# Kernel tuning notes

Hardware: AMD Instinct MI355X
Metric: run time of the kernel (lower is better)

## Reference

```python
import jax, jax.numpy as jnp
import numpy as np

B, N, D = 4, 2048, 512
H, DH = 8, 64
MLP = 2048
EPS = 1e-5


def setup_inputs() -> dict:
    key = jax.random.key(0)
    ks = jax.random.split(key, 8)
    s = lambda fan_in: 1.0 / np.sqrt(fan_in)
    return {
        "x": jax.random.normal(ks[0], (B, N, D), jnp.float32),
        "ln1_g": jnp.ones((D,), jnp.float32),
        "ln1_b": jnp.zeros((D,), jnp.float32),
        "Wqkv": jax.random.normal(ks[1], (D, 3 * H * DH), jnp.float32) * s(D),
        "temperature": jnp.asarray(np.log(DH ** -0.5), jnp.float32),
        "Wo": jax.random.normal(ks[2], (H * DH, D), jnp.float32) * s(H * DH),
        "bo": jnp.zeros((D,), jnp.float32),
        "ln2_g": jnp.ones((D,), jnp.float32),
        "ln2_b": jnp.zeros((D,), jnp.float32),
        "W1": jax.random.normal(ks[3], (D, MLP), jnp.float32) * s(D),
        "b1": jnp.zeros((MLP,), jnp.float32),
        "W2": jax.random.normal(ks[4], (MLP, D), jnp.float32) * s(MLP),
        "b2": jnp.zeros((D,), jnp.float32),
    }


def _layernorm(x, g, b):
    mu = jnp.mean(x, axis=-1, keepdims=True)
    var = jnp.var(x, axis=-1, keepdims=True)
    return (x - mu) * jax.lax.rsqrt(var + EPS) * g + b


def _lsa(x, Wqkv, temperature, Wo, bo):
    b, n, _ = x.shape
    qkv = x @ Wqkv  # [b, n, 3*H*DH]
    q, k, v = jnp.split(qkv, 3, axis=-1)
    rs = lambda t: t.reshape(b, n, H, DH).transpose(0, 2, 1, 3)  # b h n d
    q, k, v = rs(q), rs(k), rs(v)
    dots = jnp.einsum("bhnd,bhmd->bhnm", q, k) * jnp.exp(temperature)
    mask_value = -jnp.finfo(dots.dtype).max
    eye = jnp.eye(n, dtype=bool)
    dots = jnp.where(eye, mask_value, dots)  # mask diagonal (LSA)
    attn = jax.nn.softmax(dots, axis=-1)
    out = jnp.einsum("bhnm,bhmd->bhnd", attn, v)
    out = out.transpose(0, 2, 1, 3).reshape(b, n, H * DH)
    return out @ Wo + bo


def _ffn(x, W1, b1, W2, b2):
    h = jax.nn.gelu(x @ W1 + b1, approximate=False)
    return h @ W2 + b2


def reference(x, ln1_g, ln1_b, Wqkv, temperature, Wo, bo,
              ln2_g, ln2_b, W1, b1, W2, b2):
    y = _lsa(_layernorm(x, ln1_g, ln1_b), Wqkv, temperature, Wo, bo) + x
    z = _ffn(_layernorm(y, ln2_g, ln2_b), W1, b1, W2, b2) + y
    return (z, x)
```

## Files before the change

### kernel.cpp

```cpp
#include <hip/hip_runtime.h>
#include <math.h>

typedef __attribute__((ext_vector_type(4))) float f32x4;
typedef __attribute__((ext_vector_type(8))) short short8;

#define DEV __device__ __forceinline__

DEV short f2bf(float f){
  union { float f; unsigned u; } v; v.f = f;
  unsigned r = v.u + 0x7fffu + ((v.u >> 16) & 1u);
  return (short)(r >> 16);
}
DEV float bf2f(short s){
  union { unsigned u; float f; } v; v.u = ((unsigned)(unsigned short)s) << 16; return v.f;
}
DEV float exp2_hw(float x){ float r; asm("v_exp_f32 %0, %1" : "=v"(r) : "v"(x)); return r; }
DEV float rcp_hw(float x){ float r; asm("v_rcp_f32 %0, %1" : "=v"(r) : "v"(x)); return r; }
DEV unsigned cvtpk(float a, float b){
  unsigned r; asm("v_cvt_pk_bf16_f32 %0, %1, %2" : "=v"(r) : "v"(a), "v"(b)); return r;
}
DEV void gload_lds16(const short* src, short* lds){
  __builtin_amdgcn_global_load_lds(
      (const __attribute__((address_space(1))) void*)src,
      (__attribute__((address_space(3))) void*)lds, 16, 0, 0);
}

__global__ __launch_bounds__(256) void transpose_bf16_kernel(
    const float* __restrict__ W, short* __restrict__ Wt, int K, int N)
{
  __shared__ float tile[32][33];
  int nb = blockIdx.x * 32, kb = blockIdx.y * 32;
  int tx = threadIdx.x & 31, ty = threadIdx.x >> 5;
  #pragma unroll
  for (int i = ty; i < 32; i += 8)
    tile[i][tx] = W[(size_t)(kb + i) * N + nb + tx];
  __syncthreads();
  #pragma unroll
  for (int i = ty; i < 32; i += 8)
    Wt[(size_t)(nb + i) * K + kb + tx] = f2bf(tile[tx][i]);
}

template<int COPYX>
__global__ __launch_bounds__(256) void ln_kernel(
    const float* __restrict__ x, const float* __restrict__ g,
    const float* __restrict__ b, short* __restrict__ out,
    float* __restrict__ xcopy)
{
  int row  = blockIdx.x * 4 + (threadIdx.x >> 6);
  int lane = threadIdx.x & 63;
  const float* xr = x + (size_t)row * 512 + lane * 8;
  f32x4 v0 = *(const f32x4*)(xr);
  f32x4 v1 = *(const f32x4*)(xr + 4);
  float s  = (v0[0]+v0[1]+v0[2]+v0[3]) + (v1[0]+v1[1]+v1[2]+v1[3]);
  float sq = (v0[0]*v0[0]+v0[1]*v0[1]+v0[2]*v0[2]+v0[3]*v0[3])
           + (v1[0]*v1[0]+v1[1]*v1[1]+v1[2]*v1[2]+v1[3]*v1[3]);
  #pragma unroll
  for (int off = 1; off < 64; off <<= 1) {
    s  += __shfl_xor(s, off);
    sq += __shfl_xor(sq, off);
  }
  float mu  = s * (1.0f / 512.0f);
  float var = sq * (1.0f / 512.0f) - mu * mu;
  float rstd = rsqrtf(var + 1e-5f);
  f32x4 g0 = *(const f32x4*)(g + lane * 8);
  f32x4 g1 = *(const f32x4*)(g + lane * 8 + 4);
  f32x4 b0 = *(const f32x4*)(b + lane * 8);
  f32x4 b1 = *(const f32x4*)(b + lane * 8 + 4);
  float o[8];
  #pragma unroll
  for (int j = 0; j < 4; ++j) o[j]     = (v0[j] - mu) * rstd * g0[j] + b0[j];
  #pragma unroll
  for (int j = 0; j < 4; ++j) o[4 + j] = (v1[j] - mu) * rstd * g1[j] + b1[j];
  uint4 pk;
  pk.x = cvtpk(o[0], o[1]); pk.y = cvtpk(o[2], o[3]);
  pk.z = cvtpk(o[4], o[5]); pk.w = cvtpk(o[6], o[7]);
  *(uint4*)(out + (size_t)row * 512 + lane * 8) = pk;
  if (COPYX) {
    float* xc = xcopy + (size_t)row * 512 + lane * 8;
    *(f32x4*)(xc)     = v0;
    *(f32x4*)(xc + 4) = v1;
  }
}

template<int EPI, int BM, typename OutT>
__global__ __launch_bounds__(256) void gemm_bt_kernel(
    const short* __restrict__ A, const short* __restrict__ Bt,
    OutT* __restrict__ C, const float* __restrict__ bias,
    const float* __restrict__ resid, short* __restrict__ vt,
    int M, int N, int K)
{
  constexpr int MFR = BM / 32;
  constexpr int NFR = 4;
  constexpr int AI  = BM / 64;
  constexpr int BUF = BM * 32 + 128 * 32;
  __shared__ __align__(16) short smem[3 * BUF];

  int tid = threadIdx.x;
  int lane = tid & 63, wid = tid >> 6;
  int l16 = lane & 15, lq = lane >> 4;

  int gx = gridDim.x;
  int nwg = gx * gridDim.y;
  int orig = blockIdx.y * gx + blockIdx.x;
  int swz = (orig & 7) * (nwg >> 3) + (orig >> 3);
  int bn = swz % gx, bm = swz / gx;

  int wm = wid >> 1, wn = wid & 1;

  const short* gaP[AI];
  const short* gbP[2];
  #pragma unroll
  for (int i = 0; i < AI; ++i) {
    int gg = i * 4 + wid;
    gaP[i] = A + (size_t)(bm * BM + gg * 16 + l16) * K + lq * 8;
  }
  #pragma unroll
  for (int i = 0; i < 2; ++i) {
    int gg = i * 4 + wid;
    gbP[i] = Bt + (size_t)(bn * 128 + gg * 16 + l16) * K + lq * 8;
  }

  auto STAGE = [&](int bufi, int k0) {
    short* base = smem + bufi * BUF;
    #pragma unroll
    for (int i = 0; i < AI; ++i)
      gload_lds16(gaP[i] + k0, base + (i * 4 + wid) * 512);
    #pragma unroll
    for (int i = 0; i < 2; ++i)
      gload_lds16(gbP[i] + k0, base + BM * 32 + (i * 4 + wid) * 512);
  };

  f32x4 acc[MFR][NFR] = {};

  STAGE(0, 0);
  STAGE(1, 32);

  int nt = K >> 5;
  for (int t = 0; t < nt; ++t) {
    if (t + 1 < nt) {
      if constexpr (AI == 2) asm volatile("s_waitcnt vmcnt(4)" ::: "memory");
      else                   asm volatile("s_waitcnt vmcnt(3)" ::: "memory");
    } else {
      asm volatile("s_waitcnt vmcnt(0)" ::: "memory");
    }
    __builtin_amdgcn_s_barrier();
    __builtin_amdgcn_sched_barrier(0);
    if (t + 2 < nt) STAGE((t + 2) % 3, (t + 2) << 5);

    const short* base = smem + (t % 3) * BUF;
    short8 af[MFR], bfr[NFR];
    #pragma unroll
    for (int m = 0; m < MFR; ++m)
      af[m] = *(const short8*)(base + (wm * MFR + m) * 512 + lane * 8);
    #pragma unroll
    for (int n = 0; n < NFR; ++n)
      bfr[n] = *(const short8*)(base + BM * 32 + (wn * NFR + n) * 512 + lane * 8);
    __builtin_amdgcn_s_setprio(1);
    #pragma unroll
    for (int m = 0; m < MFR; ++m)
      #pragma unroll
      for (int n = 0; n < NFR; ++n)
        acc[m][n] = __builtin_amdgcn_mfma_f32_16x16x32_bf16(af[m], bfr[n], acc[m][n], 0, 0, 0);
    __builtin_amdgcn_s_setprio(0);
  }

  if (EPI == 3 && bn >= 8) {
    __syncthreads();
    short* T = smem;
    #pragma unroll
    for (int m = 0; m < MFR; ++m)
      #pragma unroll
      for (int n = 0; n < NFR; ++n) {
        int c = wn * 64 + n * 16 + l16;
        #pragma unroll
        for (int r = 0; r < 4; ++r) {
          int rowl = wm * 64 + m * 16 + lq * 4 + r;
          T[c * 128 + (rowl ^ ((c & 7) << 4))] = f2bf(acc[m][n][r]);
        }
      }
    __syncthreads();
    int b2 = bm >> 4;
    int nnb = (bm & 15) * 128;
    int tn = tid & 15;
    #pragma unroll
    for (int c8 = 0; c8 < 8; ++c8) {
      int c = c8 * 16 + (tid >> 4);
      short8 v = *(const short8*)(T + c * 128 + ((tn * 8) ^ ((c & 7) << 4)));
      if (tn & 1) {
        short8 w;
        #pragma unroll
        for (int j = 0; j < 8; ++j) w[j] = v[j ^ 4];
        v = w;
      }
      int c2 = bn * 128 + c - 1024;
      int bh = b2 * 8 + (c2 >> 6);
      int d  = c2 & 63;
      *(short8*)(vt + ((size_t)(bh * 64 + d)) * 2048 + nnb + tn * 8) = v;
    }
    return;
  }

  float bv[NFR];
  #pragma unroll
  for (int n = 0; n < NFR; ++n)
    bv[n] = (EPI == 0 || EPI == 3) ? 0.0f : bias[bn * 128 + (wn * NFR + n) * 16 + l16];

  #pragma unroll
  for (int m = 0; m < MFR; ++m) {
    #pragma unroll
    for (int r = 0; r < 4; ++r) {
      int row = bm * BM + (wm * MFR + m) * 16 + lq * 4 + r;
      #pragma unroll
      for (int n = 0; n < NFR; ++n) {
        int col = bn * 128 + (wn * NFR + n) * 16 + l16;
        float v = acc[m][n][r];
        if (EPI == 1 || EPI == 2) v += bv[n];
        if (EPI == 2) v = 0.5f * v * (1.0f + erff(v * 0.70710678f));
        if (EPI == 1) v += resid[(size_t)row * N + col];
        if constexpr (sizeof(OutT) == 2)
          ((short*)C)[(size_t)row * N + col] = f2bf(v);
        else
          ((float*)C)[(size_t)row * N + col] = v;
      }
    }
  }
}

__global__ __launch_bounds__(256, 2) void attn_kernel(
    const short* __restrict__ qkv, const short* __restrict__ vt,
    const float* __restrict__ temp_ptr, short* __restrict__ out)
{
  __shared__ __align__(16) short smem[24576];

  int tid = threadIdx.x;
  int lane = tid & 63, wid = tid >> 6;
  int l16 = lane & 15, lq = lane >> 4;
  int hi = lq >> 1, lq0 = lq & 1;

  int orig = blockIdx.y * 16 + blockIdx.x;
  int swz = (orig & 7) * 64 + (orig >> 3);
  int qb = swz & 15, bh = swz >> 4;
  int b = bh >> 3, h = bh & 7;

  const short* qbase = qkv + (size_t)b * 2048 * 1536 + h * 64;
  const short* kbase = qbase + 512;
  const short* vbase = vt + (size_t)bh * 64 * 2048;

  float scale = __expf(temp_ptr[0]) * 1.44269504f;
  int q0 = qb * 128 + wid * 32;

  short8 qfrag[2][2];
  #pragma unroll
  for (int qf = 0; qf < 2; ++qf) {
    int qrow = q0 + qf * 16 + l16;
    #pragma unroll
    for (int c = 0; c < 2; ++c) {
      short8 raw = *(const short8*)(qbase + (size_t)qrow * 1536 + c * 32 + lq * 8);
      short8 sc;
      #pragma unroll
      for (int j = 0; j < 8; ++j) sc[j] = f2bf(bf2f(raw[j]) * scale);
      qfrag[qf][c] = sc;
    }
  }

  f32x4 accO[2][4] = {};
  float l[2] = {0.f, 0.f};

  auto STAGE = [&](int bufi, int k0) {
    #pragma unroll
    for (int i = 0; i < 2; ++i) {
      int w16 = i * 256 + tid;
      int sub = w16 >> 7;
      int cc  = (w16 >> 6) & 1;
      int lq2 = (w16 >> 4) & 3;
      int l2  = w16 & 15;
      const short* srcK = kbase + (size_t)(k0 + sub * 16 + l2) * 1536 + cc * 32 + lq2 * 8;
      gload_lds16(srcK, smem + bufi * 4096 + (i * 4 + wid) * 512);
      const short* srcV = vbase + (size_t)(sub * 16 + l2) * 2048 + k0 + cc * 32 + lq2 * 8;
      gload_lds16(srcV, smem + 12288 + bufi * 4096 + (i * 4 + wid) * 512);
    }
  };

  STAGE(0, 0);
  STAGE(1, 64);

  for (int t = 0; t < 32; ++t) {
    if (t + 1 < 32) asm volatile("s_waitcnt vmcnt(4)" ::: "memory");
    else            asm volatile("s_waitcnt vmcnt(0)" ::: "memory");
    __builtin_amdgcn_s_barrier();
    __builtin_amdgcn_sched_barrier(0);
    if (t + 2 < 32) STAGE((t + 2) % 3, (t + 2) * 64);

    int k0 = t * 64;
    const short* kls = smem + (t % 3) * 4096;
    const short* vls = smem + 12288 + (t % 3) * 4096;

    f32x4 accS[2][4] = {};
    __builtin_amdgcn_s_setprio(1);
    #pragma unroll
    for (int s = 0; s < 4; ++s) {
      short8 kf0 = *(const short8*)(kls + (s * 2 + 0) * 512 + lane * 8);
      short8 kf1 = *(const short8*)(kls + (s * 2 + 1) * 512 + lane * 8);
      #pragma unroll
      for (int qf = 0; qf < 2; ++qf) {
        accS[qf][s] = __builtin_amdgcn_mfma_f32_16x16x32_bf16(kf0, qfrag[qf][0], accS[qf][s], 0, 0, 0);
        accS[qf][s] = __builtin_amdgcn_mfma_f32_16x16x32_bf16(kf1, qfrag[qf][1], accS[qf][s], 0, 0, 0);
      }
    }
    __builtin_amdgcn_s_setprio(0);

    if ((q0 & ~63) == k0) {
      #pragma unroll
      for (int qf = 0; qf < 2; ++qf) {
        int qg = q0 + qf * 16 + l16;
        #pragma unroll
        for (int s = 0; s < 4; ++s)
          #pragma unroll
          for (int r = 0; r < 4; ++r)
            if (k0 + s * 16 + lq * 4 + r == qg) accS[qf][s][r] = -30000.f;
      }
    }

    short8 pa[2][2];
    #pragma unroll
    for (int qf = 0; qf < 2; ++qf) {
      float sum = 0.f;
      unsigned W[4][2];
      #pragma unroll
      for (int s = 0; s < 4; ++s) {
        float p0 = exp2_hw(accS[qf][s][0]);
        float p1 = exp2_hw(accS[qf][s][1]);
        float p2 = exp2_hw(accS[qf][s][2]);
        float p3 = exp2_hw(accS[qf][s][3]);
        sum += (p0 + p1) + (p2 + p3);
        W[s][0] = cvtpk(p0, p1);
        W[s][1] = cvtpk(p2, p3);
      }
      sum += __shfl_xor(sum, 16);
      sum += __shfl_xor(sum, 32);
      l[qf] += sum;

      unsigned K0[2], S0[2], K2[2], S2[2], R0[2], R2[2];
      #pragma unroll
      for (int w = 0; w < 2; ++w) {
        K0[w] = hi ? W[1][w] : W[0][w];
        S0[w] = hi ? W[0][w] : W[1][w];
        K2[w] = hi ? W[3][w] : W[2][w];
        S2[w] = hi ? W[2][w] : W[3][w];
      }
      #pragma unroll
      for (int w = 0; w < 2; ++w) {
        R0[w] = (unsigned)__shfl_xor((int)S0[w], 32);
        R2[w] = (unsigned)__shfl_xor((int)S2[w], 32);
      }
      bool sw = (hi != lq0);
      unsigned FA[2], FB[2], sA[2], sB[2], GA[2], GB[2];
      #pragma unroll
      for (int w = 0; w < 2; ++w) {
        sA[w] = sw ? K0[w] : R0[w];  FA[w] = sw ? R0[w] : K0[w];
        sB[w] = sw ? K2[w] : R2[w];  FB[w] = sw ? R2[w] : K2[w];
      }
      #pragma unroll
      for (int w = 0; w < 2; ++w) {
        GA[w] = (unsigned)__shfl_xor((int)sA[w], 16);
        GB[w] = (unsigned)__shfl_xor((int)sB[w], 16);
      }
      union { unsigned u[4]; short8 s8; } p0u, p1u;
      p0u.u[0] = FA[0]; p0u.u[1] = FA[1]; p0u.u[2] = GA[0]; p0u.u[3] = GA[1];
      p1u.u[0] = FB[0]; p1u.u[1] = FB[1]; p1u.u[2] = GB[0]; p1u.u[3] = GB[1];
      pa[qf][0] = p0u.s8;
      pa[qf][1] = p1u.s8;
    }

    short8 vfr[4][2];
    #pragma unroll
    for (int d = 0; d < 4; ++d) {
      vfr[d][0] = *(const short8*)(vls + (d * 2 + 0) * 512 + lane * 8);
      vfr[d][1] = *(const short8*)(vls + (d * 2 + 1) * 512 + lane * 8);
    }
    __builtin_amdgcn_s_setprio(1);
    #pragma unroll
    for (int qf = 0; qf < 2; ++qf)
      #pragma unroll
      for (int d = 0; d < 4; ++d) {
        accO[qf][d] = __builtin_amdgcn_mfma_f32_16x16x32_bf16(vfr[d][0], pa[qf][0], accO[qf][d], 0, 0, 0);
        accO[qf][d] = __builtin_amdgcn_mfma_f32_16x16x32_bf16(vfr[d][1], pa[qf][1], accO[qf][d], 0, 0, 0);
      }
    __builtin_amdgcn_s_setprio(0);
  }

  #pragma unroll
  for (int qf = 0; qf < 2; ++qf) {
    float inv = rcp_hw(l[qf]);
    int qg = q0 + qf * 16 + l16;
    size_t rowoff = (size_t)(b * 2048 + qg) * 512 + h * 64;
    #pragma unroll
    for (int d = 0; d < 4; ++d) {
      unsigned w0 = cvtpk(accO[qf][d][0] * inv, accO[qf][d][1] * inv);
      unsigned w1 = cvtpk(accO[qf][d][2] * inv, accO[qf][d][3] * inv);
      uint2 pk; pk.x = w0; pk.y = w1;
      *(uint2*)(out + rowoff + d * 16 + lq * 4) = pk;
    }
  }
}

extern "C" void kernel_launch(void* const* d_in, const int* in_sizes, int n_in,
                              void* d_out, int out_size, void* d_ws, size_t ws_size,
                              hipStream_t stream)
{
  const float* x    = (const float*)d_in[0];
  const float* ln1g = (const float*)d_in[1];
  const float* ln1b = (const float*)d_in[2];
  const float* Wqkv = (const float*)d_in[3];
  const float* temp = (const float*)d_in[4];
  const float* Wo   = (const float*)d_in[5];
  const float* bo   = (const float*)d_in[6];
  const float* ln2g = (const float*)d_in[7];
  const float* ln2b = (const float*)d_in[8];
  const float* W1   = (const float*)d_in[9];
  const float* b1   = (const float*)d_in[10];
  const float* W2   = (const float*)d_in[11];
  const float* b2   = (const float*)d_in[12];
  float* out = (float*)d_out;

  char* ws = (char*)d_ws;
  short* wqkv_t = (short*)(ws);
  short* wo_t   = (short*)(ws + 1572864);
  short* w1_t   = (short*)(ws + 2097152);
  short* w2_t   = (short*)(ws + 4194304);
  short* h      = (short*)(ws + 6291456);
  short* qkv    = (short*)(ws + 14680064);
  short* attn   = (short*)(ws + 39845888);
  float* y      = (float*)(ws + 48234496);
  short* vt     = (short*)(ws + 48234496);
  short* t      = (short*)(ws + 14680064);

  const int M = 8192;

  transpose_bf16_kernel<<<dim3(1536 / 32, 512 / 32),  256, 0, stream>>>(Wqkv, wqkv_t, 512, 1536);
  transpose_bf16_kernel<<<dim3(512 / 32, 512 / 32),   256, 0, stream>>>(Wo,   wo_t,   512, 512);
  transpose_bf16_kernel<<<dim3(2048 / 32, 512 / 32),  256, 0, stream>>>(W1,   w1_t,   512, 2048);
  transpose_bf16_kernel<<<dim3(512 / 32, 2048 / 32),  256, 0, stream>>>(W2,   w2_t,   2048, 512);

  ln_kernel<1><<<M / 4, 256, 0, stream>>>(x, ln1g, ln1b, h, out + (size_t)M * 512);

  gemm_bt_kernel<3, 128, short><<<dim3(1536 / 128, M / 128), 256, 0, stream>>>(
      h, wqkv_t, qkv, nullptr, nullptr, vt, M, 1536, 512);

  attn_kernel<<<dim3(16, 32), 256, 0, stream>>>(qkv, vt, temp, attn);

  gemm_bt_kernel<1, 64, float><<<dim3(512 / 128, M / 64), 256, 0, stream>>>(
      attn, wo_t, y, bo, x, nullptr, M, 512, 512);

  ln_kernel<0><<<M / 4, 256, 0, stream>>>(y, ln2g, ln2b, h, nullptr);

  gemm_bt_kernel<2, 128, short><<<dim3(2048 / 128, M / 128), 256, 0, stream>>>(
      h, w1_t, t, b1, nullptr, nullptr, M, 2048, 512);

  gemm_bt_kernel<1, 64, float><<<dim3(512 / 128, M / 64), 256, 0, stream>>>(
      t, w2_t, out, b2, y, nullptr, M, 512, 2048);
}
```

Before: 223.9 us.

## Split attention keys across two slices, use bf16 residual stream and tanh GELU

The attention kernel now splits the 2048 keys into two halves, doubling the grid. Each half writes unnormalized partial outputs and row sums, and a new combine kernel merges them. The intent is better CU occupancy, at the cost of an extra pass over the partial outputs and lower precision from rounding the partials to bf16. The post-attention residual y is also stored in bf16 instead of fp32, and LN2 reads the bf16 copy; this cuts memory traffic but loses precision. The exact erf GELU is replaced by a tanh approximation built on hardware exp and reciprocal, and the attention loop drops from triple to double buffering and no longer sets wave priority.

```diff
diff --git a/kernel.cpp b/kernel.cpp
--- a/kernel.cpp
+++ b/kernel.cpp
@@ -23,6 +23,12 @@
   __builtin_amdgcn_global_load_lds(
       (const __attribute__((address_space(1))) void*)src,
       (__attribute__((address_space(3))) void*)lds, 16, 0, 0);
+}
+DEV float gelu_fast(float v){
+  float u = v * (0.79788456f + 0.03567741f * v * v);
+  float e = exp2_hw(u * 2.88539008f);
+  float th = 1.0f - 2.0f * rcp_hw(e + 1.0f);
+  return 0.5f * v * (1.0f + th);
 }
 
 __global__ __launch_bounds__(256) void transpose_bf16_kernel(
@@ -82,12 +88,48 @@
   }
 }
 
+__global__ __launch_bounds__(256) void ln_bf_kernel(
+    const short* __restrict__ x, const float* __restrict__ g,
+    const float* __restrict__ b, short* __restrict__ out)
+{
+  int row  = blockIdx.x * 4 + (threadIdx.x >> 6);
+  int lane = threadIdx.x & 63;
+  short8 raw = *(const short8*)(x + (size_t)row * 512 + lane * 8);
+  float v[8];
+  #pragma unroll
+  for (int j = 0; j < 8; ++j) v[j] = bf2f(raw[j]);
+  float s = 0.f, sq = 0.f;
+  #pragma unroll
+  for (int j = 0; j < 8; ++j) { s += v[j]; sq += v[j] * v[j]; }
+  #pragma unroll
+  for (int off = 1; off < 64; off <<= 1) {
+    s  += __shfl_xor(s, off);
+    sq += __shfl_xor(sq, off);
+  }
+  float mu  = s * (1.0f / 512.0f);
+  float var = sq * (1.0f / 512.0f) - mu * mu;
+  float rstd = rsqrtf(var + 1e-5f);
+  f32x4 g0 = *(const f32x4*)(g + lane * 8);
+  f32x4 g1 = *(const f32x4*)(g + lane * 8 + 4);
+  f32x4 b0 = *(const f32x4*)(b + lane * 8);
+  f32x4 b1 = *(const f32x4*)(b + lane * 8 + 4);
+  float o[8];
+  #pragma unroll
+  for (int j = 0; j < 4; ++j) o[j]     = (v[j] - mu) * rstd * g0[j] + b0[j];
+  #pragma unroll
+  for (int j = 0; j < 4; ++j) o[4 + j] = (v[4+j] - mu) * rstd * g1[j] + b1[j];
+  uint4 pk;
+  pk.x = cvtpk(o[0], o[1]); pk.y = cvtpk(o[2], o[3]);
+  pk.z = cvtpk(o[4], o[5]); pk.w = cvtpk(o[6], o[7]);
+  *(uint4*)(out + (size_t)row * 512 + lane * 8) = pk;
+}
+
 template<int EPI, int BM, typename OutT>
 __global__ __launch_bounds__(256) void gemm_bt_kernel(
     const short* __restrict__ A, const short* __restrict__ Bt,
     OutT* __restrict__ C, const float* __restrict__ bias,
-    const float* __restrict__ resid, short* __restrict__ vt,
-    int M, int N, int K)
+    const float* __restrict__ resid, const short* __restrict__ residb,
+    short* __restrict__ vt, int M, int N, int K)
 {
   constexpr int MFR = BM / 32;
   constexpr int NFR = 4;
@@ -214,9 +256,10 @@
       for (int n = 0; n < NFR; ++n) {
         int col = bn * 128 + (wn * NFR + n) * 16 + l16;
         float v = acc[m][n][r];
-        if (EPI == 1 || EPI == 2) v += bv[n];
-        if (EPI == 2) v = 0.5f * v * (1.0f + erff(v * 0.70710678f));
-        if (EPI == 1) v += resid[(size_t)row * N + col];
+        if (EPI == 2 || EPI == 4 || EPI == 5) v += bv[n];
+        if (EPI == 2) v = gelu_fast(v);
+        if (EPI == 4) v += resid[(size_t)row * N + col];
+        if (EPI == 5) v += bf2f(residb[(size_t)row * N + col]);
         if constexpr (sizeof(OutT) == 2)
           ((short*)C)[(size_t)row * N + col] = f2bf(v);
         else
@@ -228,9 +271,10 @@
 
 __global__ __launch_bounds__(256, 2) void attn_kernel(
     const short* __restrict__ qkv, const short* __restrict__ vt,
-    const float* __restrict__ temp_ptr, short* __restrict__ out)
-{
-  __shared__ __align__(16) short smem[24576];
+    const float* __restrict__ temp_ptr,
+    short* __restrict__ Op0, short* __restrict__ Op1, float* __restrict__ Lbuf)
+{
+  __shared__ __align__(16) short smem[16384];
 
   int tid = threadIdx.x;
   int lane = tid & 63, wid = tid >> 6;
@@ -238,13 +282,16 @@
   int hi = lq >> 1, lq0 = lq & 1;
 
   int orig = blockIdx.y * 16 + blockIdx.x;
-  int swz = (orig & 7) * 64 + (orig >> 3);
-  int qb = swz & 15, bh = swz >> 4;
+  int swz = (orig & 7) * 128 + (orig >> 3);
+  int qb = swz & 15;
+  int rr = swz >> 4;
+  int bh = rr & 31, slice = rr >> 5;
   int b = bh >> 3, h = bh & 7;
 
   const short* qbase = qkv + (size_t)b * 2048 * 1536 + h * 64;
   const short* kbase = qbase + 512;
   const short* vbase = vt + (size_t)bh * 64 * 2048;
+  int kslice = slice * 1024;
 
   float scale = __expf(temp_ptr[0]) * 1.44269504f;
   int q0 = qb * 128 + wid * 32;
@@ -277,26 +324,23 @@
       const short* srcK = kbase + (size_t)(k0 + sub * 16 + l2) * 1536 + cc * 32 + lq2 * 8;
       gload_lds16(srcK, smem + bufi * 4096 + (i * 4 + wid) * 512);
       const short* srcV = vbase + (size_t)(sub * 16 + l2) * 2048 + k0 + cc * 32 + lq2 * 8;
-      gload_lds16(srcV, smem + 12288 + bufi * 4096 + (i * 4 + wid) * 512);
+      gload_lds16(srcV, smem + 8192 + bufi * 4096 + (i * 4 + wid) * 512);
     }
   };
 
-  STAGE(0, 0);
-  STAGE(1, 64);
-
-  for (int t = 0; t < 32; ++t) {
-    if (t + 1 < 32) asm volatile("s_waitcnt vmcnt(4)" ::: "memory");
-    else            asm volatile("s_waitcnt vmcnt(0)" ::: "memory");
-    __builtin_amdgcn_s_barrier();
-    __builtin_amdgcn_sched_barrier(0);
-    if (t + 2 < 32) STAGE((t + 2) % 3, (t + 2) * 64);
-
-    int k0 = t * 64;
-    const short* kls = smem + (t % 3) * 4096;
-    const short* vls = smem + 12288 + (t % 3) * 4096;
+  STAGE(0, kslice);
+  asm volatile("s_waitcnt vmcnt(0)");
+  __syncthreads();
+
+  for (int t = 0; t < 16; ++t) {
+    int cur = t & 1;
+    int k0 = kslice + t * 64;
+    if (t + 1 < 16) STAGE(cur ^ 1, k0 + 64);
+
+    const short* kls = smem + cur * 4096;
+    const short* vls = smem + 8192 + cur * 4096;
 
     f32x4 accS[2][4] = {};
-    __builtin_amdgcn_s_setprio(1);
     #pragma unroll
     for (int s = 0; s < 4; ++s) {
       short8 kf0 = *(const short8*)(kls + (s * 2 + 0) * 512 + lane * 8);
@@ -307,7 +351,6 @@
         accS[qf][s] = __builtin_amdgcn_mfma_f32_16x16x32_bf16(kf1, qfrag[qf][1], accS[qf][s], 0, 0, 0);
       }
     }
-    __builtin_amdgcn_s_setprio(0);
 
     if ((q0 & ~63) == k0) {
       #pragma unroll
@@ -378,7 +421,6 @@
       vfr[d][0] = *(const short8*)(vls + (d * 2 + 0) * 512 + lane * 8);
       vfr[d][1] = *(const short8*)(vls + (d * 2 + 1) * 512 + lane * 8);
     }
-    __builtin_amdgcn_s_setprio(1);
     #pragma unroll
     for (int qf = 0; qf < 2; ++qf)
       #pragma unroll
@@ -386,22 +428,48 @@
         accO[qf][d] = __builtin_amdgcn_mfma_f32_16x16x32_bf16(vfr[d][0], pa[qf][0], accO[qf][d], 0, 0, 0);
         accO[qf][d] = __builtin_amdgcn_mfma_f32_16x16x32_bf16(vfr[d][1], pa[qf][1], accO[qf][d], 0, 0, 0);
       }
-    __builtin_amdgcn_s_setprio(0);
-  }
-
+
+    __syncthreads();
+  }
+
+  short* op = slice ? Op1 : Op0;
   #pragma unroll
   for (int qf = 0; qf < 2; ++qf) {
-    float inv = rcp_hw(l[qf]);
     int qg = q0 + qf * 16 + l16;
+    if (lq == 0) Lbuf[(size_t)(slice * 32 + bh) * 2048 + qg] = l[qf];
     size_t rowoff = (size_t)(b * 2048 + qg) * 512 + h * 64;
     #pragma unroll
     for (int d = 0; d < 4; ++d) {
-      unsigned w0 = cvtpk(accO[qf][d][0] * inv, accO[qf][d][1] * inv);
-      unsigned w1 = cvtpk(accO[qf][d][2] * inv, accO[qf][d][3] * inv);
+      unsigned w0 = cvtpk(accO[qf][d][0], accO[qf][d][1]);
+      unsigned w1 = cvtpk(accO[qf][d][2], accO[qf][d][3]);
       uint2 pk; pk.x = w0; pk.y = w1;
-      *(uint2*)(out + rowoff + d * 16 + lq * 4) = pk;
-    }
-  }
+      *(uint2*)(op + rowoff + d * 16 + lq * 4) = pk;
+    }
+  }
+}
+
+__global__ __launch_bounds__(256) void attn_combine_kernel(
+    const short* __restrict__ Op0, const short* __restrict__ Op1,
+    const float* __restrict__ Lbuf, short* __restrict__ out)
+{
+  int idx = blockIdx.x * 256 + threadIdx.x;
+  size_t e = (size_t)idx * 8;
+  int row = (int)(e >> 9);
+  int col = (int)(e & 511);
+  int b = row >> 11, q = row & 2047;
+  int bh = b * 8 + (col >> 6);
+  float l0 = Lbuf[(size_t)bh * 2048 + q];
+  float l1 = Lbuf[(size_t)(32 + bh) * 2048 + q];
+  float inv = rcp_hw(l0 + l1);
+  short8 a = *(const short8*)(Op0 + e);
+  short8 c = *(const short8*)(Op1 + e);
+  float o[8];
+  #pragma unroll
+  for (int j = 0; j < 8; ++j) o[j] = (bf2f(a[j]) + bf2f(c[j])) * inv;
+  uint4 pk;
+  pk.x = cvtpk(o[0], o[1]); pk.y = cvtpk(o[2], o[3]);
+  pk.z = cvtpk(o[4], o[5]); pk.w = cvtpk(o[6], o[7]);
+  *(uint4*)(out + e) = pk;
 }
 
 extern "C" void kernel_launch(void* const* d_in, const int* in_sizes, int n_in,
@@ -425,13 +493,14 @@
 
   char* ws = (char*)d_ws;
   short* wqkv_t = (short*)(ws);
+  float* lpart  = (float*)(ws);
   short* wo_t   = (short*)(ws + 1572864);
   short* w1_t   = (short*)(ws + 2097152);
   short* w2_t   = (short*)(ws + 4194304);
   short* h      = (short*)(ws + 6291456);
   short* qkv    = (short*)(ws + 14680064);
   short* attn   = (short*)(ws + 39845888);
-  float* y      = (float*)(ws + 48234496);
+  short* ybf    = (short*)(ws + 48234496);
   short* vt     = (short*)(ws + 48234496);
   short* t      = (short*)(ws + 14680064);
 
@@ -445,18 +514,19 @@
   ln_kernel<1><<<M / 4, 256, 0, stream>>>(x, ln1g, ln1b, h, out + (size_t)M * 512);
 
   gemm_bt_kernel<3, 128, short><<<dim3(1536 / 128, M / 128), 256, 0, stream>>>(
-      h, wqkv_t, qkv, nullptr, nullptr, vt, M, 1536, 512);
-
-  attn_kernel<<<dim3(16, 32), 256, 0, stream>>>(qkv, vt, temp, attn);
-
-  gemm_bt_kernel<1, 64, float><<<dim3(512 / 128, M / 64), 256, 0, stream>>>(
-      attn, wo_t, y, bo, x, nullptr, M, 512, 512);
-
-  ln_kernel<0><<<M / 4, 256, 0, stream>>>(y, ln2g, ln2b, h, nullptr);
+      h, wqkv_t, qkv, nullptr, nullptr, nullptr, vt, M, 1536, 512);
+
+  attn_kernel<<<dim3(16, 64), 256, 0, stream>>>(qkv, vt, temp, attn, h, lpart);
+  attn_combine_kernel<<<M * 512 / 8 / 256, 256, 0, stream>>>(attn, h, lpart, attn);
+
+  gemm_bt_kernel<4, 64, short><<<dim3(512 / 128, M / 64), 256, 0, stream>>>(
+      attn, wo_t, ybf, bo, x, nullptr, nullptr, M, 512, 512);
+
+  ln_bf_kernel<<<M / 4, 256, 0, stream>>>(ybf, ln2g, ln2b, h);
 
   gemm_bt_kernel<2, 128, short><<<dim3(2048 / 128, M / 128), 256, 0, stream>>>(
-      h, w1_t, t, b1, nullptr, nullptr, M, 2048, 512);
-
-  gemm_bt_kernel<1, 64, float><<<dim3(512 / 128, M / 64), 256, 0, stream>>>(
-      t, w2_t, out, b2, y, nullptr, M, 512, 2048);
-}
+      h, w1_t, t, b1, nullptr, nullptr, nullptr, M, 2048, 512);
+
+  gemm_bt_kernel<5, 64, float><<<dim3(512 / 128, M / 64), 256, 0, stream>>>(
+      t, w2_t, out, b2, nullptr, ybf, nullptr, M, 512, 2048);
+}
```

New measurement: 210.1 us. 1.07x faster.
